# Performance work log

Hardware: AMD Instinct MI355X
Metric: run time of the kernel (lower is better)

Reference implementation:

```python
import jax, jax.numpy as jnp
import numpy as np

K_NEIGHBORS = 20


def _glorot(key, shape):
    fan_in = shape[0]
    return jax.random.normal(key, shape, dtype=jnp.float32) / jnp.sqrt(jnp.float32(fan_in))


def setup_inputs() -> dict:
    key = jax.random.key(0)
    ks = jax.random.split(key, 20)
    B, N, D = 16, 1024, 3
    out_channels = 40
    pos = jax.random.normal(ks[0], (B, N, D), dtype=jnp.float32)
    inp = {
        "pos": pos,
        # conv1 MLP: [6 -> 64 -> 64 -> 64]
        "W1a": _glorot(ks[1], (6, 64)),   "b1a": jnp.zeros((64,), jnp.float32),
        "W1b": _glorot(ks[2], (64, 64)),  "b1b": jnp.zeros((64,), jnp.float32),
        "W1c": _glorot(ks[3], (64, 64)),  "b1c": jnp.zeros((64,), jnp.float32),
        # conv2 MLP: [128 -> 128]
        "W2": _glorot(ks[4], (128, 128)), "b2": jnp.zeros((128,), jnp.float32),
        # lin1: 64+128 -> 1024
        "Wl": _glorot(ks[5], (192, 1024)), "bl": jnp.zeros((1024,), jnp.float32),
        # head MLP: [1024 -> 512 -> 256 -> out]
        "Wm1": _glorot(ks[6], (1024, 512)), "bm1": jnp.zeros((512,), jnp.float32),
        "Wm2": _glorot(ks[7], (512, 256)),  "bm2": jnp.zeros((256,), jnp.float32),
        "Wm3": _glorot(ks[8], (256, out_channels)), "bm3": jnp.zeros((out_channels,), jnp.float32),
    }
    return inp


def _knn_idx(x, k):
    # x: [B, N, D] -> idx: [B, N, k] of nearest neighbors (self excluded)
    sq = jnp.sum(x * x, axis=-1)                      # [B, N]
    d = sq[:, :, None] + sq[:, None, :] - 2.0 * jnp.einsum("bnd,bmd->bnm", x, x)
    n = x.shape[1]
    d = d + jnp.eye(n, dtype=d.dtype)[None] * jnp.float32(1e10)  # exclude self
    _, idx = jax.lax.top_k(-d, k)                     # smallest distances
    return idx


def _edge_conv(x, k, mlp_fn):
    # DynamicEdgeConv: kNN graph on current features, message = mlp([x_i, x_j - x_i]), max-aggr.
    idx = _knn_idx(x, k)                              # [B, N, k]
    nb = jax.vmap(lambda xb, ib: xb[ib])(x, idx)      # [B, N, k, C] gather
    xi = jnp.broadcast_to(x[:, :, None, :], nb.shape)
    e = jnp.concatenate([xi, nb - xi], axis=-1)       # [B, N, k, 2C]
    return jnp.max(mlp_fn(e), axis=2)                 # max over neighbors -> [B, N, C']


def reference(pos, W1a, b1a, W1b, b1b, W1c, b1c, W2, b2, Wl, bl,
              Wm1, bm1, Wm2, bm2, Wm3, bm3):
    relu = jax.nn.relu
    # conv1: MLP([6,64,64,64]) -- ReLU after hidden layers, plain last (eval: BN identity, dropout off)
    mlp1 = lambda e: relu(relu(e @ W1a + b1a) @ W1b + b1b) @ W1c + b1c
    x1 = _edge_conv(pos, K_NEIGHBORS, mlp1)           # [B, N, 64]
    # conv2: MLP([128,128]) -- single plain linear
    x2 = _edge_conv(x1, K_NEIGHBORS, lambda e: e @ W2 + b2)  # [B, N, 128]
    out = jnp.concatenate([x1, x2], axis=-1) @ Wl + bl       # [B, N, 1024]
    g = jnp.max(out, axis=1)                                  # global max pool -> [B, 1024]
    h = relu(g @ Wm1 + bm1)
    h = relu(h @ Wm2 + bm2)
    logits = h @ Wm3 + bm3                                    # [B, 40]
    return jax.nn.log_softmax(logits, axis=1)
```

## Files before the change

### kernel.cpp

```cpp
#include <hip/hip_runtime.h>

constexpr int NB  = 16;
constexpr int NP  = 1024;
constexpr int NPT = NB * NP;
constexpr int KNB = 20;

typedef unsigned short ushortT;
typedef __bf16 bf16x8 __attribute__((ext_vector_type(8)));
typedef _Float16 f16x8 __attribute__((ext_vector_type(8)));
typedef float f32x4 __attribute__((ext_vector_type(4)));

__device__ inline unsigned f2bf_pair(float f0, float f1) {
    unsigned u0 = __float_as_uint(f0); u0 = (u0 + 0x7FFFu + ((u0 >> 16) & 1u)) >> 16;
    unsigned u1 = __float_as_uint(f1); u1 = (u1 + 0x7FFFu + ((u1 >> 16) & 1u)) >> 16;
    return u0 | (u1 << 16);
}

__device__ inline unsigned monokey(float f) {
    unsigned u = __float_as_uint(f);
    return u ^ ((unsigned)((int)u >> 31) | 0x80000000u);
}

__device__ inline unsigned dppmin16(unsigned v) {
    unsigned t;
    t = (unsigned)__builtin_amdgcn_update_dpp((int)v, (int)v, 0xB1, 0xF, 0xF, false);
    v = v < t ? v : t;
    t = (unsigned)__builtin_amdgcn_update_dpp((int)v, (int)v, 0x4E, 0xF, 0xF, false);
    v = v < t ? v : t;
    t = (unsigned)__builtin_amdgcn_update_dpp((int)v, (int)v, 0x141, 0xF, 0xF, false);
    v = v < t ? v : t;
    t = (unsigned)__builtin_amdgcn_update_dpp((int)v, (int)v, 0x140, 0xF, 0xF, false);
    v = v < t ? v : t;
    return v;
}

__device__ inline void sort16_u64(unsigned long long key[16]) {
#pragma unroll
    for (int k = 2; k <= 16; k <<= 1) {
#pragma unroll
        for (int j = k >> 1; j > 0; j >>= 1) {
#pragma unroll
            for (int a = 0; a < 16; ++a) {
                int b = a ^ j;
                if (b > a) {
                    unsigned long long x = key[a], y = key[b];
                    bool lt = x < y;
                    unsigned long long mn = lt ? x : y, mx = lt ? y : x;
                    if ((a & k) == 0) { key[a] = mn; key[b] = mx; }
                    else              { key[a] = mx; key[b] = mn; }
                }
            }
        }
    }
}

__device__ inline void wave_top20_lds(unsigned long long key[16], int lane,
                                      unsigned long long* __restrict__ col,
                                      int* __restrict__ outp, int jadd)
{
    sort16_u64(key);
#pragma unroll
    for (int s = 0; s < 16; ++s) col[s] = key[s];
    unsigned ptr = 0;
    unsigned long long cur = col[0];
    unsigned long long nxt = col[1];
    for (int t = 0; t < KNB; ++t) {
        unsigned hv = (unsigned)(cur >> 32);
        unsigned hj = (unsigned)cur;
        unsigned r = dppmin16(hv);
        unsigned g0 = (unsigned)__builtin_amdgcn_readlane((int)r, 0);
        unsigned g1 = (unsigned)__builtin_amdgcn_readlane((int)r, 16);
        unsigned g2 = (unsigned)__builtin_amdgcn_readlane((int)r, 32);
        unsigned g3 = (unsigned)__builtin_amdgcn_readlane((int)r, 48);
        unsigned g = min(min(g0, g1), min(g2, g3));
        unsigned long long ball = __ballot(hv == g);
        int wl = __ffsll(ball) - 1;
        int wj = __builtin_amdgcn_readlane((int)hj, wl);
        if (lane == 0) outp[t] = jadd + wj;
        if (lane == wl) {
            cur = nxt;
            ptr += 1u;
            unsigned p2 = ptr + 1u;
            unsigned p2c = p2 < 15u ? p2 : 15u;
            unsigned long long ld = col[p2c];
            nxt = (p2 < 16u) ? ld : ~0ULL;
        }
    }
}

__global__ void fail_kernel(float* out, int n) {
    int i = blockIdx.x * 256 + threadIdx.x;
    if (i < n) out[i] = -777.0f;
}

__global__ __launch_bounds__(256) void phase1_kernel(
    const float* __restrict__ pos, const float* __restrict__ W1a, const float* __restrict__ b1a,
    const float* __restrict__ W2,
    const float* __restrict__ Wm1, const float* __restrict__ Wm2, const float* __restrict__ Wm3,
    const float* __restrict__ Wl, const float* __restrict__ W1b, const float* __restrict__ W1c,
    int* __restrict__ idx, float* __restrict__ u1, float* __restrict__ v1,
    float* __restrict__ Wcat, float* __restrict__ Wm1T, float* __restrict__ Wm2T, float* __restrict__ Wm3T,
    ushortT* __restrict__ Wlb, _Float16* __restrict__ Wc1f)
{
    __shared__ unsigned long long heap[4][64][16];
    const int bid = blockIdx.x;
    const int tid = threadIdx.x;
    if (bid < 4096) {
        const int w = tid >> 6, lane = tid & 63;
        const int b = bid >> 8;
        const int i = ((bid & 255) << 2) + w;
        const float* pb = pos + (size_t)b * NP * 3;
        float cbuf[48];
        {
            const float4* src = (const float4*)(pb + lane * 48);
#pragma unroll
            for (int q = 0; q < 12; ++q) *(float4*)&cbuf[q * 4] = src[q];
        }
        const float xi = pb[3 * i], yi = pb[3 * i + 1], zi = pb[3 * i + 2];
        const float sqi = xi * xi + yi * yi + zi * zi;
        unsigned long long key[16];
#pragma unroll
        for (int s = 0; s < 16; ++s) {
            float x = cbuf[3 * s], y = cbuf[3 * s + 1], z = cbuf[3 * s + 2];
            float d = sqi + (x * x + y * y + z * z) - 2.0f * (xi * x + yi * y + zi * z);
            int j = (lane << 4) + s;
            if (j == i) d += 1e10f;
            key[s] = ((unsigned long long)monokey(d) << 32) | (unsigned)j;
        }
        wave_top20_lds(key, lane, &heap[w][lane][0], idx + (size_t)(b * NP + i) * KNB, b * NP);
        return;
    }
    if (bid < 8192) {
        int id = (bid - 4096) * 256 + tid;
        int i = id >> 6, c = id & 63;
        float x = pos[3 * i], y = pos[3 * i + 1], z = pos[3 * i + 2];
        float wu0 = W1a[3 * 64 + c], wu1 = W1a[4 * 64 + c], wu2 = W1a[5 * 64 + c];
        float wv0 = W1a[0 * 64 + c] - wu0, wv1 = W1a[1 * 64 + c] - wu1, wv2 = W1a[2 * 64 + c] - wu2;
        u1[id] = x * wu0 + y * wu1 + z * wu2;
        v1[id] = b1a[c] + x * wv0 + y * wv1 + z * wv2;
        return;
    }
    int id = (bid - 8192) * 256 + tid;
    if (id < 64 * 256) {
        int c = id >> 8, n = id & 255;
        float wb = W2[(64 + c) * 128 + (n & 127)];
        Wcat[id] = (n < 128) ? wb : (W2[c * 128 + (n - 128)] - wb);
        return;
    }
    id -= 64 * 256;
    if (id < 512 * 1024) { int j = id >> 10, c = id & 1023; Wm1T[id] = Wm1[c * 512 + j]; return; }
    id -= 512 * 1024;
    if (id < 256 * 512)  { int j = id >> 9,  c = id & 511;  Wm2T[id] = Wm2[c * 256 + j]; return; }
    id -= 256 * 512;
    if (id < 40 * 256)   { int j = id >> 8,  c = id & 255;  Wm3T[id] = Wm3[c * 40 + j];  return; }
    id -= 40 * 256;
    if (id < 8 * 6 * 8 * 64 * 8) {
        int j = id & 7;
        int t = id >> 3;
        int lane = t & 63; t >>= 6;
        int f = t & 7; t >>= 3;
        int s = t % 6, nt = t / 6;
        int k = s * 32 + (lane >> 4) * 8 + j;
        int n = nt * 128 + f * 16 + (lane & 15);
        unsigned u = __float_as_uint(Wl[(size_t)k * 1024 + n]);
        u = (u + 0x7FFFu + ((u >> 16) & 1u)) >> 16;
        Wlb[id] = (ushortT)u;
        return;
    }
    id -= 8 * 6 * 8 * 64 * 8;
    if (id < 16384) {
        int mat = id >> 13;
        int rem = id & 8191;
        int part = rem >> 12;
        int t = rem & 4095;
        int frag = t >> 9;
        int r = t & 511;
        int lane = r >> 3, j = r & 7;
        int kf = frag >> 2, nf = frag & 3;
        int k = kf * 32 + (lane >> 4) * 8 + j;
        int n = nf * 16 + (lane & 15);
        float w = (mat ? W1c : W1b)[k * 64 + n];
        _Float16 hi = (_Float16)w;
        Wc1f[id] = part ? (_Float16)(w - (float)hi) : hi;
        return;
    }
}

__global__ __launch_bounds__(64, 1) void conv1_mfma_kernel(
    const int* __restrict__ idx, const float* __restrict__ u1, const float* __restrict__ v1,
    const _Float16* __restrict__ Wf, const float* __restrict__ b1b, const float* __restrict__ b1c,
    float* __restrict__ x1)
{
    __shared__ int idx_s[16 * 20];
    __shared__ __align__(16) float tr[16 * 68];
    __shared__ __align__(16) float xout[16 * 68];
    const int lane = threadIdx.x;
    const int row = lane & 15, ks = lane >> 4;
    const int pbase = blockIdx.x * 16;

    for (int t = lane; t < 320; t += 64) idx_s[t] = idx[(size_t)pbase * 20 + t];

    const f16x8* Wp = (const f16x8*)Wf;
    f16x8 wbh[2][4], wbl[2][4], wch[2][4], wcl[2][4];
#pragma unroll
    for (int kf = 0; kf < 2; ++kf)
#pragma unroll
        for (int nf = 0; nf < 4; ++nf) {
            int f = kf * 4 + nf;
            wbh[kf][nf] = Wp[(0 * 8 + f) * 64 + lane];
            wbl[kf][nf] = Wp[(1 * 8 + f) * 64 + lane];
            wch[kf][nf] = Wp[(2 * 8 + f) * 64 + lane];
            wcl[kf][nf] = Wp[(3 * 8 + f) * 64 + lane];
        }
    float bb[4], bc[4];
#pragma unroll
    for (int nf = 0; nf < 4; ++nf) { bb[nf] = b1b[nf * 16 + row]; bc[nf] = b1c[nf * 16 + row]; }

    const int P = pbase + row;
    float4 v1f[4];
    {
        const float4* v4a = (const float4*)(v1 + (size_t)P * 64 + ks * 8);
        v1f[0] = v4a[0]; v1f[1] = v4a[1];
        const float4* v4b = (const float4*)(v1 + (size_t)P * 64 + 32 + ks * 8);
        v1f[2] = v4b[0]; v1f[3] = v4b[1];
    }
    f32x4 xmax[4];
#pragma unroll
    for (int nf = 0; nf < 4; ++nf) xmax[nf] = (f32x4)(-3.0e38f);

    int jn = idx_s[row * 20];
    float4 un[4];
    {
        const float4* up = (const float4*)(u1 + (size_t)jn * 64 + ks * 8);
        un[0] = up[0]; un[1] = up[1];
        const float4* up2 = (const float4*)(u1 + (size_t)jn * 64 + 32 + ks * 8);
        un[2] = up2[0]; un[3] = up2[1];
    }
    for (int e = 0; e < 20; ++e) {
        float4 uc[4] = {un[0], un[1], un[2], un[3]};
        if (e < 19) {
            jn = idx_s[row * 20 + e + 1];
            const float4* up = (const float4*)(u1 + (size_t)jn * 64 + ks * 8);
            un[0] = up[0]; un[1] = up[1];
            const float4* up2 = (const float4*)(u1 + (size_t)jn * 64 + 32 + ks * 8);
            un[2] = up2[0]; un[3] = up2[1];
        }
        f32x4 c2[4];
#pragma unroll
        for (int nf = 0; nf < 4; ++nf) c2[nf] = (f32x4)(bb[nf]);
#pragma unroll
        for (int kf = 0; kf < 2; ++kf) {
            const float* uu = (const float*)&uc[kf * 2];
            const float* vv = (const float*)&v1f[kf * 2];
            f16x8 ah, al;
#pragma unroll
            for (int q = 0; q < 8; ++q) {
                float h = fmaxf(uu[q] + vv[q], 0.f);
                _Float16 hi = (_Float16)h;
                ah[q] = hi;
                al[q] = (_Float16)(h - (float)hi);
            }
#pragma unroll
            for (int nf = 0; nf < 4; ++nf) {
                c2[nf] = __builtin_amdgcn_mfma_f32_16x16x32_f16(ah, wbh[kf][nf], c2[nf], 0, 0, 0);
                c2[nf] = __builtin_amdgcn_mfma_f32_16x16x32_f16(ah, wbl[kf][nf], c2[nf], 0, 0, 0);
                c2[nf] = __builtin_amdgcn_mfma_f32_16x16x32_f16(al, wbh[kf][nf], c2[nf], 0, 0, 0);
            }
        }
#pragma unroll
        for (int nf = 0; nf < 4; ++nf)
#pragma unroll
            for (int r = 0; r < 4; ++r)
                tr[(ks * 4 + r) * 68 + nf * 16 + row] = fmaxf(c2[nf][r], 0.f);
        __builtin_amdgcn_sched_barrier(0);
        f32x4 c3[4];
#pragma unroll
        for (int nf = 0; nf < 4; ++nf) c3[nf] = (f32x4)0.0f;
#pragma unroll
        for (int kf = 0; kf < 2; ++kf) {
            float hbuf[8];
            *(float4*)&hbuf[0] = *(const float4*)&tr[row * 68 + kf * 32 + ks * 8];
            *(float4*)&hbuf[4] = *(const float4*)&tr[row * 68 + kf * 32 + ks * 8 + 4];
            f16x8 ah, al;
#pragma unroll
            for (int q = 0; q < 8; ++q) {
                _Float16 hi = (_Float16)hbuf[q];
                ah[q] = hi;
                al[q] = (_Float16)(hbuf[q] - (float)hi);
            }
#pragma unroll
            for (int nf = 0; nf < 4; ++nf) {
                c3[nf] = __builtin_amdgcn_mfma_f32_16x16x32_f16(ah, wch[kf][nf], c3[nf], 0, 0, 0);
                c3[nf] = __builtin_amdgcn_mfma_f32_16x16x32_f16(ah, wcl[kf][nf], c3[nf], 0, 0, 0);
                c3[nf] = __builtin_amdgcn_mfma_f32_16x16x32_f16(al, wch[kf][nf], c3[nf], 0, 0, 0);
            }
        }
        __builtin_amdgcn_sched_barrier(0);
#pragma unroll
        for (int nf = 0; nf < 4; ++nf) {
            xmax[nf][0] = fmaxf(xmax[nf][0], c3[nf][0]);
            xmax[nf][1] = fmaxf(xmax[nf][1], c3[nf][1]);
            xmax[nf][2] = fmaxf(xmax[nf][2], c3[nf][2]);
            xmax[nf][3] = fmaxf(xmax[nf][3], c3[nf][3]);
        }
    }
#pragma unroll
    for (int nf = 0; nf < 4; ++nf)
#pragma unroll
        for (int r = 0; r < 4; ++r)
            xout[(ks * 4 + r) * 68 + nf * 16 + row] = xmax[nf][r] + bc[nf];
    __builtin_amdgcn_sched_barrier(0);
    {
        const int r2 = lane >> 2, c0 = (lane & 3) * 16;
#pragma unroll
        for (int q = 0; q < 4; ++q) {
            float4 v = *(const float4*)&xout[r2 * 68 + c0 + q * 4];
            *(float4*)(x1 + (size_t)(pbase + r2) * 64 + c0 + q * 4) = v;
        }
    }
}

__global__ __launch_bounds__(256) void sqnorm_kernel(
    const float* __restrict__ x1, float* __restrict__ sq,
    ushortT* __restrict__ Afrag, _Float16* __restrict__ Xf)
{
    int i = blockIdx.x * 256 + threadIdx.x;
    const float4* r = (const float4*)(x1 + (size_t)i * 64);
    float c[64];
    float s = 0.f;
#pragma unroll
    for (int q = 0; q < 16; ++q) {
        float4 a = r[q];
        c[4 * q] = a.x; c[4 * q + 1] = a.y; c[4 * q + 2] = a.z; c[4 * q + 3] = a.w;
        s += a.x * a.x + a.y * a.y + a.z * a.z + a.w * a.w;
    }
    sq[i] = s;
    const size_t t = i >> 4;
#pragma unroll
    for (int cb = 0; cb < 8; ++cb) {
        uint4 pk;
        pk.x = f2bf_pair(c[8 * cb + 0], c[8 * cb + 1]);
        pk.y = f2bf_pair(c[8 * cb + 2], c[8 * cb + 3]);
        pk.z = f2bf_pair(c[8 * cb + 4], c[8 * cb + 5]);
        pk.w = f2bf_pair(c[8 * cb + 6], c[8 * cb + 7]);
        size_t af = (t * 6 + (cb >> 2)) * 512 + (size_t)((cb & 3) * 16 + (i & 15)) * 8;
        *(uint4*)(Afrag + af) = pk;
        int kf = cb >> 2;
        int lanef = ((cb & 3) << 4) + (i & 15);
        __align__(16) _Float16 hbuf[8];
        __align__(16) _Float16 lbuf[8];
#pragma unroll
        for (int q2 = 0; q2 < 8; ++q2) {
            float v = c[cb * 8 + q2];
            _Float16 hi = (_Float16)v;
            hbuf[q2] = hi;
            lbuf[q2] = (_Float16)(v - (float)hi);
        }
        *(uint4*)(Xf + ((t * 2 + kf) * 2 + 0) * 512 + (size_t)lanef * 8) = *(uint4*)hbuf;
        *(uint4*)(Xf + ((t * 2 + kf) * 2 + 1) * 512 + (size_t)lanef * 8) = *(uint4*)lbuf;
    }
}

__global__ __launch_bounds__(512, 2) void dist2sel_kernel(
    const _Float16* __restrict__ Xf, const float* __restrict__ sq, int* __restrict__ idx)
{
    __shared__ unsigned kls[16 * 1024];
    const int tid = threadIdx.x;
    const int w = tid >> 6, lane = tid & 63;
    const int b = blockIdx.x >> 6;
    const int rowtile = blockIdx.x & 63;
    const int c15 = lane & 15;
    const int rbase = (lane >> 4) * 4;

    const f16x8* Xv = (const f16x8*)Xf;
    const int tA = b * 64 + rowtile;
    f16x8 ah[2], al[2];
#pragma unroll
    for (int kf = 0; kf < 2; ++kf) {
        ah[kf] = Xv[((size_t)(tA * 2 + kf) * 2 + 0) * 64 + lane];
        al[kf] = Xv[((size_t)(tA * 2 + kf) * 2 + 1) * 64 + lane];
    }
    const float* sqb = sq + (size_t)b * NP;
    float sqi[4];
#pragma unroll
    for (int rr = 0; rr < 4; ++rr)
        sqi[rr] = sqb[rowtile * 16 + rbase + rr];

    for (int q = 0; q < 8; ++q) {
        const int ct = w * 8 + q;
        const int tB = b * 64 + ct;
        f16x8 bh0 = Xv[((size_t)(tB * 2 + 0) * 2 + 0) * 64 + lane];
        f16x8 bl0 = Xv[((size_t)(tB * 2 + 0) * 2 + 1) * 64 + lane];
        f16x8 bh1 = Xv[((size_t)(tB * 2 + 1) * 2 + 0) * 64 + lane];
        f16x8 bl1 = Xv[((size_t)(tB * 2 + 1) * 2 + 1) * 64 + lane];
        const int col = ct * 16 + c15;
        const float sqj = sqb[col];
        f32x4 acc = (f32x4)0.0f;
        acc = __builtin_amdgcn_mfma_f32_16x16x32_f16(ah[0], bh0, acc, 0, 0, 0);
        acc = __builtin_amdgcn_mfma_f32_16x16x32_f16(ah[0], bl0, acc, 0, 0, 0);
        acc = __builtin_amdgcn_mfma_f32_16x16x32_f16(al[0], bh0, acc, 0, 0, 0);
        acc = __builtin_amdgcn_mfma_f32_16x16x32_f16(ah[1], bh1, acc, 0, 0, 0);
        acc = __builtin_amdgcn_mfma_f32_16x16x32_f16(ah[1], bl1, acc, 0, 0, 0);
        acc = __builtin_amdgcn_mfma_f32_16x16x32_f16(al[1], bh1, acc, 0, 0, 0);
        const int pc = col ^ ((col >> 6) & 15);
#pragma unroll
        for (int rr = 0; rr < 4; ++rr) {
            float d = sqi[rr] + sqj - 2.0f * acc[rr];
            if (rowtile * 16 + rbase + rr == col) d += 1e10f;
            kls[(rbase + rr) * 1024 + pc] = monokey(d);
        }
    }
    __syncthreads();

    const int gb = b * NP;
    const int r0 = 2 * w, r1 = 2 * w + 1;
    unsigned* hrow0 = &kls[r0 * 1024];
    unsigned* hrow1 = &kls[r1 * 1024];
    unsigned long long perm0 = 0, perm1 = 0;
    {
        unsigned long long key[16];
#pragma unroll
        for (int s = 0; s < 16; ++s) {
            int col = (lane << 4) + s;
            int pc = col ^ ((col >> 6) & 15);
            key[s] = ((unsigned long long)kls[r0 * 1024 + pc] << 32) | (unsigned)col;
        }
        sort16_u64(key);
#pragma unroll
        for (int p = 0; p < 16; ++p) {
            hrow0[p * 64 + lane] = (unsigned)(key[p] >> 32);
            perm0 |= (unsigned long long)((unsigned)key[p] & 15u) << (4 * p);
        }
    }
    {
        unsigned long long key[16];
#pragma unroll
        for (int s = 0; s < 16; ++s) {
            int col = (lane << 4) + s;
            int pc = col ^ ((col >> 6) & 15);
            key[s] = ((unsigned long long)kls[r1 * 1024 + pc] << 32) | (unsigned)col;
        }
        sort16_u64(key);
#pragma unroll
        for (int p = 0; p < 16; ++p) {
            hrow1[p * 64 + lane] = (unsigned)(key[p] >> 32);
            perm1 |= (unsigned long long)((unsigned)key[p] & 15u) << (4 * p);
        }
    }
    unsigned ptrA = 0, ptrB = 0;
    unsigned curA = hrow0[lane], nxtA = hrow0[64 + lane];
    unsigned curB = hrow1[lane], nxtB = hrow1[64 + lane];
    unsigned csA = (unsigned)(perm0 & 15ull), nsA = (unsigned)((perm0 >> 4) & 15ull);
    unsigned csB = (unsigned)(perm1 & 15ull), nsB = (unsigned)((perm1 >> 4) & 15ull);
    int* outA = idx + (size_t)(gb + rowtile * 16 + r0) * KNB;
    int* outB = idx + (size_t)(gb + rowtile * 16 + r1) * KNB;
    for (int t = 0; t < KNB; ++t) {
        unsigned rmA = dppmin16(curA);
        unsigned rmB = dppmin16(curB);
        unsigned a0 = (unsigned)__builtin_amdgcn_readlane((int)rmA, 0);
        unsigned b0 = (unsigned)__builtin_amdgcn_readlane((int)rmB, 0);
        unsigned a1 = (unsigned)__builtin_amdgcn_readlane((int)rmA, 16);
        unsigned b1 = (unsigned)__builtin_amdgcn_readlane((int)rmB, 16);
        unsigned a2 = (unsigned)__builtin_amdgcn_readlane((int)rmA, 32);
        unsigned b2 = (unsigned)__builtin_amdgcn_readlane((int)rmB, 32);
        unsigned a3 = (unsigned)__builtin_amdgcn_readlane((int)rmA, 48);
        unsigned b3 = (unsigned)__builtin_amdgcn_readlane((int)rmB, 48);
        unsigned gA = min(min(a0, a1), min(a2, a3));
        unsigned gB = min(min(b0, b1), min(b2, b3));
        unsigned long long ballA = __ballot(curA == gA);
        unsigned long long ballB = __ballot(curB == gB);
        int wlA = __ffsll(ballA) - 1;
        int wlB = __ffsll(ballB) - 1;
        int jA = (lane << 4) + (int)csA;
        int jB = (lane << 4) + (int)csB;
        int wjA = __builtin_amdgcn_readlane(jA, wlA);
        int wjB = __builtin_amdgcn_readlane(jB, wlB);
        if (lane == 0) { outA[t] = gb + wjA; outB[t] = gb + wjB; }
        if (lane == wlA) {
            curA = nxtA; csA = nsA;
            ptrA += 1u;
            unsigned p2 = ptrA + 1u;
            unsigned p2c = p2 < 15u ? p2 : 15u;
            nsA = (unsigned)((perm0 >> (4 * (int)p2c)) & 15ull);
            nxtA = (p2 < 16u) ? hrow0[p2 * 64 + lane] : 0xFFFFFFFFu;
        }
        if (lane == wlB) {
            curB = nxtB; csB = nsB;
            ptrB += 1u;
            unsigned p2 = ptrB + 1u;
            unsigned p2c = p2 < 15u ? p2 : 15u;
            nsB = (unsigned)((perm1 >> (4 * (int)p2c)) & 15ull);
            nxtB = (p2 < 16u) ? hrow1[p2 * 64 + lane] : 0xFFFFFFFFu;
        }
    }
}

__global__ __launch_bounds__(256) void u2v2_kernel(
    const float* __restrict__ x1, const float* __restrict__ Wcat, const float* __restrict__ b2,
    float* __restrict__ u2, float* __restrict__ v2)
{
    __shared__ float aT[32][132];
    __shared__ float bW[32][132];
    const int tid = threadIdx.x;
    const int mt = blockIdx.x >> 1, nt = blockIdx.x & 1;
    const int m0 = mt << 7, n0 = nt << 7;
    const int ti = tid >> 4, tj = tid & 15;
    float acc[8][8];
#pragma unroll
    for (int a = 0; a < 8; ++a)
#pragma unroll
        for (int q = 0; q < 8; ++q) acc[a][q] = 0.f;
    for (int ct = 0; ct < 2; ++ct) {
        __syncthreads();
#pragma unroll
        for (int rep = 0; rep < 4; ++rep) {
            int f = tid + (rep << 8);
            { int r = f >> 3, q = f & 7;
              float4 v = *(const float4*)(x1 + (size_t)(m0 + r) * 64 + ct * 32 + q * 4);
              aT[4 * q + 0][r] = v.x; aT[4 * q + 1][r] = v.y; aT[4 * q + 2][r] = v.z; aT[4 * q + 3][r] = v.w; }
            { int cc = f >> 5, q = f & 31;
              *(float4*)&bW[cc][4 * q] = *(const float4*)(Wcat + (size_t)(ct * 32 + cc) * 256 + n0 + q * 4); }
        }
        __syncthreads();
#pragma unroll 4
        for (int c = 0; c < 32; ++c) {
            float af[8], bf[8];
            *(float4*)&af[0] = *(const float4*)&aT[c][ti * 8];
            *(float4*)&af[4] = *(const float4*)&aT[c][ti * 8 + 4];
            *(float4*)&bf[0] = *(const float4*)&bW[c][tj * 8];
            *(float4*)&bf[4] = *(const float4*)&bW[c][tj * 8 + 4];
#pragma unroll
            for (int a = 0; a < 8; ++a)
#pragma unroll
                for (int q = 0; q < 8; ++q) acc[a][q] = fmaf(af[a], bf[q], acc[a][q]);
        }
    }
#pragma unroll
    for (int a = 0; a < 8; ++a) {
        int m = m0 + ti * 8 + a;
        if (n0 < 128) {
            float outv[8];
#pragma unroll
            for (int q = 0; q < 8; ++q) outv[q] = acc[a][q];
            *(float4*)(u2 + (size_t)m * 128 + n0 + tj * 8)     = *(float4*)&outv[0];
            *(float4*)(u2 + (size_t)m * 128 + n0 + tj * 8 + 4) = *(float4*)&outv[4];
        } else {
            float outv[8];
#pragma unroll
            for (int q = 0; q < 8; ++q) outv[q] = acc[a][q] + b2[n0 - 128 + tj * 8 + q];
            *(float4*)(v2 + (size_t)m * 128 + (n0 - 128) + tj * 8)     = *(float4*)&outv[0];
            *(float4*)(v2 + (size_t)m * 128 + (n0 - 128) + tj * 8 + 4) = *(float4*)&outv[4];
        }
    }
}

__global__ __launch_bounds__(256) void gatherfrag_kernel(
    const int* __restrict__ idx, const float* __restrict__ u2,
    const float* __restrict__ v2, ushortT* __restrict__ Afrag)
{
    const int tid = threadIdx.x;
    const int i = blockIdx.x * 16 + (tid >> 4);
    const int cb = tid & 15;
    const int* ib = idx + (size_t)i * KNB;
    float m[8];
#pragma unroll
    for (int d = 0; d < 8; ++d) m[d] = -3e38f;
    for (int e = 0; e < KNB; ++e) {
        int j = ib[e];
        const float4* p = (const float4*)(u2 + (size_t)j * 128 + cb * 8);
        float4 a = p[0], b = p[1];
        m[0] = fmaxf(m[0], a.x); m[1] = fmaxf(m[1], a.y); m[2] = fmaxf(m[2], a.z); m[3] = fmaxf(m[3], a.w);
        m[4] = fmaxf(m[4], b.x); m[5] = fmaxf(m[5], b.y); m[6] = fmaxf(m[6], b.z); m[7] = fmaxf(m[7], b.w);
    }
    const float4* vp = (const float4*)(v2 + (size_t)i * 128 + cb * 8);
    float4 va = vp[0], vb = vp[1];
    m[0] += va.x; m[1] += va.y; m[2] += va.z; m[3] += va.w;
    m[4] += vb.x; m[5] += vb.y; m[6] += vb.z; m[7] += vb.w;
    uint4 pk;
    pk.x = f2bf_pair(m[0], m[1]);
    pk.y = f2bf_pair(m[2], m[3]);
    pk.z = f2bf_pair(m[4], m[5]);
    pk.w = f2bf_pair(m[6], m[7]);
    size_t af = ((size_t)(i >> 4) * 6 + 2 + (cb >> 2)) * 512 + (size_t)((cb & 3) * 16 + (i & 15)) * 8;
    *(uint4*)(Afrag + af) = pk;
}

__global__ __launch_bounds__(256) void lin1max_mfma_kernel(
    const ushortT* __restrict__ Afrag, const ushortT* __restrict__ Wlb, float* __restrict__ gp)
{
    __shared__ float red[4][128];
    const int tid = threadIdx.x;
    const int w = tid >> 6, lane = tid & 63;
    const int nt = blockIdx.x & 7;
    const int rt = (blockIdx.x >> 3) & 7;
    const int b  = blockIdx.x >> 6;
    const int rt16 = ((b << 3) + rt) * 8 + (w << 1);
    const bf16x8* Ap = (const bf16x8*)Afrag;
    const bf16x8* Bp = (const bf16x8*)Wlb;
    f32x4 acc[2][8];
#pragma unroll
    for (int mm = 0; mm < 2; ++mm)
#pragma unroll
        for (int f = 0; f < 8; ++f) acc[mm][f] = (f32x4)0.0f;
#pragma unroll
    for (int s = 0; s < 6; ++s) {
        bf16x8 a0 = Ap[((rt16    ) * 6 + s) * 64 + lane];
        bf16x8 a1 = Ap[((rt16 + 1) * 6 + s) * 64 + lane];
#pragma unroll
        for (int f = 0; f < 8; ++f) {
            bf16x8 bb = Bp[(((nt * 6 + s) << 3) + f) * 64 + lane];
            acc[0][f] = __builtin_amdgcn_mfma_f32_16x16x32_bf16(a0, bb, acc[0][f], 0, 0, 0);
            acc[1][f] = __builtin_amdgcn_mfma_f32_16x16x32_bf16(a1, bb, acc[1][f], 0, 0, 0);
        }
    }
#pragma unroll
    for (int f = 0; f < 8; ++f) {
        float m = acc[0][f][0];
        m = fmaxf(m, acc[0][f][1]); m = fmaxf(m, acc[0][f][2]); m = fmaxf(m, acc[0][f][3]);
        m = fmaxf(m, acc[1][f][0]); m = fmaxf(m, acc[1][f][1]);
        m = fmaxf(m, acc[1][f][2]); m = fmaxf(m, acc[1][f][3]);
        m = fmaxf(m, __shfl_xor(m, 16, 64));
        m = fmaxf(m, __shfl_xor(m, 32, 64));
        if (lane < 16) red[w][f * 16 + lane] = m;
    }
    __syncthreads();
    if (tid < 128) {
        float m = fmaxf(fmaxf(red[0][tid], red[1][tid]), fmaxf(red[2][tid], red[3][tid]));
        gp[((size_t)rt * NB + b) * 1024 + nt * 128 + tid] = m;
    }
}

__global__ __launch_bounds__(256) void gmax_kernel(
    const float* __restrict__ gp, const float* __restrict__ bl, float* __restrict__ gs)
{
    int id = blockIdx.x * 256 + threadIdx.x;
    int b = id >> 10, c = id & 1023;
    float m = gp[(size_t)b * 1024 + c];
#pragma unroll
    for (int part = 1; part < 8; ++part)
        m = fmaxf(m, gp[((size_t)part * NB + b) * 1024 + c]);
    gs[(size_t)b * 1024 + c] = m + bl[c];
}

__global__ __launch_bounds__(256) void head1_kernel(
    const float* __restrict__ gs, const float* __restrict__ Wm1T, const float* __restrict__ bm1,
    float* __restrict__ h1)
{
    __shared__ float red[16][17];
    const int j = blockIdx.x;
    const int t = threadIdx.x;
    const int b = t >> 4, seg = t & 15;
    const float4* wr = (const float4*)(Wm1T + (size_t)j * 1024 + seg * 64);
    const float4* gr = (const float4*)(gs + (size_t)b * 1024 + seg * 64);
    float acc = 0.f;
#pragma unroll
    for (int q = 0; q < 16; ++q) {
        float4 w = wr[q], g = gr[q];
        acc = fmaf(w.x, g.x, acc); acc = fmaf(w.y, g.y, acc);
        acc = fmaf(w.z, g.z, acc); acc = fmaf(w.w, g.w, acc);
    }
    red[b][seg] = acc;
    __syncthreads();
    if (t < 16) {
        float s = 0.f;
#pragma unroll
        for (int k = 0; k < 16; ++k) s += red[t][k];
        h1[(size_t)t * 512 + j] = fmaxf(s + bm1[j], 0.f);
    }
}

__global__ __launch_bounds__(256) void head2_kernel(
    const float* __restrict__ h1, const float* __restrict__ Wm2T, const float* __restrict__ bm2,
    float* __restrict__ h2)
{
    __shared__ float red[16][17];
    const int j = blockIdx.x;
    const int t = threadIdx.x;
    const int b = t >> 4, seg = t & 15;
    const float4* wr = (const float4*)(Wm2T + (size_t)j * 512 + seg * 32);
    const float4* hr = (const float4*)(h1 + (size_t)b * 512 + seg * 32);
    float acc = 0.f;
#pragma unroll
    for (int q = 0; q < 8; ++q) {
        float4 w = wr[q], g = hr[q];
        acc = fmaf(w.x, g.x, acc); acc = fmaf(w.y, g.y, acc);
        acc = fmaf(w.z, g.z, acc); acc = fmaf(w.w, g.w, acc);
    }
    red[b][seg] = acc;
    __syncthreads();
    if (t < 16) {
        float s = 0.f;
#pragma unroll
        for (int k = 0; k < 16; ++k) s += red[t][k];
        h2[(size_t)t * 256 + j] = fmaxf(s + bm2[j], 0.f);
    }
}

__global__ __launch_bounds__(256) void head3_kernel(
    const float* __restrict__ h2, const float* __restrict__ Wm3T, const float* __restrict__ bm3,
    float* __restrict__ out)
{
    __shared__ float lg[64];
    const int tid = threadIdx.x;
    const int b = blockIdx.x;
    if (tid < 40) {
        float acc = bm3[tid];
        const float4* wr = (const float4*)(Wm3T + (size_t)tid * 256);
        const float4* hr = (const float4*)(h2 + (size_t)b * 256);
#pragma unroll
        for (int c4 = 0; c4 < 64; ++c4) {
            float4 w = wr[c4];
            float4 g4 = hr[c4];
            acc = fmaf(w.x, g4.x, acc); acc = fmaf(w.y, g4.y, acc);
            acc = fmaf(w.z, g4.z, acc); acc = fmaf(w.w, g4.w, acc);
        }
        lg[tid] = acc;
    }
    __syncthreads();
    if (tid < 64) {
        float v = (tid < 40) ? lg[tid] : -3e38f;
        float m = v;
        for (int off = 32; off; off >>= 1) m = fmaxf(m, __shfl_xor(m, off, 64));
        float ex = (tid < 40) ? expf(v - m) : 0.f;
        float s = ex;
        for (int off = 32; off; off >>= 1) s += __shfl_xor(s, off, 64);
        if (tid < 40) out[b * 40 + tid] = v - m - logf(s);
    }
}

extern "C" void kernel_launch(void* const* d_in, const int* in_sizes, int n_in,
                              void* d_out, int out_size, void* d_ws, size_t ws_size,
                              hipStream_t stream)
{
    const float* pos = (const float*)d_in[0];
    const float* W1a = (const float*)d_in[1];
    const float* b1a = (const float*)d_in[2];
    const float* W1b = (const float*)d_in[3];
    const float* b1b = (const float*)d_in[4];
    const float* W1c = (const float*)d_in[5];
    const float* b1c = (const float*)d_in[6];
    const float* W2  = (const float*)d_in[7];
    const float* b2  = (const float*)d_in[8];
    const float* Wl  = (const float*)d_in[9];
    const float* bl  = (const float*)d_in[10];
    const float* Wm1 = (const float*)d_in[11];
    const float* bm1 = (const float*)d_in[12];
    const float* Wm2 = (const float*)d_in[13];
    const float* bm2 = (const float*)d_in[14];
    const float* Wm3 = (const float*)d_in[15];
    const float* bm3 = (const float*)d_in[16];
    float* out = (float*)d_out;

    char* ws = (char*)d_ws;
    const size_t MB = 1024 * 1024;
    size_t off = 0;
    auto alloc = [&](size_t bytes) { size_t o = off; off += (bytes + 255) & ~(size_t)255; return o; };
    size_t u2_off  = alloc(8 * MB);
    size_t v2_off  = alloc(8 * MB);
    size_t x1_off  = alloc(4 * MB);
    size_t idx_off = alloc((size_t)NPT * KNB * 4);
    size_t sq_off  = alloc((size_t)NPT * 4);
    size_t gp_off  = alloc((size_t)8 * NB * 1024 * 4);
    size_t gs_off  = alloc((size_t)NB * 1024 * 4);
    size_t h1_off  = alloc((size_t)NB * 512 * 4);
    size_t h2_off  = alloc((size_t)NB * 256 * 4);
    size_t wc_off  = alloc(64 * 256 * 4);
    size_t w1t_off = alloc(512 * 1024 * 4);
    size_t w2t_off = alloc(256 * 512 * 4);
    size_t w3t_off = alloc(40 * 256 * 4);
    size_t af_off  = alloc((size_t)(NPT / 16) * 6 * 512 * 2);
    size_t wlb_off = alloc((size_t)8 * 6 * 8 * 512 * 2);
    size_t wcf_off = alloc((size_t)16384 * 2);
    size_t xf_off  = alloc((size_t)(NPT / 16) * 2 * 2 * 512 * 2);
    if (ws_size < off) { fail_kernel<<<3, 256, 0, stream>>>(out, out_size); return; }

    float* u1    = (float*)(ws + u2_off);
    float* v1    = (float*)(ws + v2_off);
    float* u2    = (float*)(ws + u2_off);
    float* v2    = (float*)(ws + v2_off);
    float* x1    = (float*)(ws + x1_off);
    int*   idx   = (int*)(ws + idx_off);
    float* sq    = (float*)(ws + sq_off);
    float* gp    = (float*)(ws + gp_off);
    float* gs    = (float*)(ws + gs_off);
    float* h1    = (float*)(ws + h1_off);
    float* h2    = (float*)(ws + h2_off);
    float* Wcat  = (float*)(ws + wc_off);
    float* Wm1T  = (float*)(ws + w1t_off);
    float* Wm2T  = (float*)(ws + w2t_off);
    float* Wm3T  = (float*)(ws + w3t_off);
    ushortT* Afrag = (ushortT*)(ws + af_off);
    ushortT* Wlb   = (ushortT*)(ws + wlb_off);
    _Float16* Wc1f = (_Float16*)(ws + wcf_off);
    _Float16* Xf   = (_Float16*)(ws + xf_off);

    phase1_kernel<<<11688, 256, 0, stream>>>(pos, W1a, b1a, W2, Wm1, Wm2, Wm3, Wl, W1b, W1c,
                                             idx, u1, v1, Wcat, Wm1T, Wm2T, Wm3T, Wlb, Wc1f);
    conv1_mfma_kernel<<<1024, 64, 0, stream>>>(idx, u1, v1, Wc1f, b1b, b1c, x1);
    sqnorm_kernel<<<64, 256, 0, stream>>>(x1, sq, Afrag, Xf);
    dist2sel_kernel<<<1024, 512, 0, stream>>>(Xf, sq, idx);
    u2v2_kernel<<<256, 256, 0, stream>>>(x1, Wcat, b2, u2, v2);
    gatherfrag_kernel<<<1024, 256, 0, stream>>>(idx, u2, v2, Afrag);
    lin1max_mfma_kernel<<<1024, 256, 0, stream>>>(Afrag, Wlb, gp);
    gmax_kernel<<<64, 256, 0, stream>>>(gp, bl, gs);
    head1_kernel<<<512, 256, 0, stream>>>(gs, Wm1T, bm1, h1);
    head2_kernel<<<256, 256, 0, stream>>>(h1, Wm2T, bm2, h2);
    head3_kernel<<<16, 256, 0, stream>>>(h2, Wm3T, bm3, out);
}
```

Measured before the change: 192.9 us.

## Reuse dual-row 32-bit tournament top-20 selection for conv1 kNN in phase1

Factors the two-row tournament top-k loop out of the conv2 selection kernel into a shared helper, dual_tourney20. The conv1 kNN part of phase1 is reworked to use it, so each wave handles two query points with 32-bit keys plus a packed 4-bit column permutation instead of 64-bit keys, and the kNN section needs half as many blocks. This aims to cut the serial per-wave selection cost and the LDS traffic in the first kNN. The cost is more register use per wave for two rows, and a different tie-break path.

```diff
diff --git a/kernel.cpp b/kernel.cpp
--- a/kernel.cpp
+++ b/kernel.cpp
@@ -54,406 +54,16 @@
     }
 }
 
-__device__ inline void wave_top20_lds(unsigned long long key[16], int lane,
-                                      unsigned long long* __restrict__ col,
-                                      int* __restrict__ outp, int jadd)
-{
-    sort16_u64(key);
-#pragma unroll
-    for (int s = 0; s < 16; ++s) col[s] = key[s];
-    unsigned ptr = 0;
-    unsigned long long cur = col[0];
-    unsigned long long nxt = col[1];
-    for (int t = 0; t < KNB; ++t) {
-        unsigned hv = (unsigned)(cur >> 32);
-        unsigned hj = (unsigned)cur;
-        unsigned r = dppmin16(hv);
-        unsigned g0 = (unsigned)__builtin_amdgcn_readlane((int)r, 0);
-        unsigned g1 = (unsigned)__builtin_amdgcn_readlane((int)r, 16);
-        unsigned g2 = (unsigned)__builtin_amdgcn_readlane((int)r, 32);
-        unsigned g3 = (unsigned)__builtin_amdgcn_readlane((int)r, 48);
-        unsigned g = min(min(g0, g1), min(g2, g3));
-        unsigned long long ball = __ballot(hv == g);
-        int wl = __ffsll(ball) - 1;
-        int wj = __builtin_amdgcn_readlane((int)hj, wl);
-        if (lane == 0) outp[t] = jadd + wj;
-        if (lane == wl) {
-            cur = nxt;
-            ptr += 1u;
-            unsigned p2 = ptr + 1u;
-            unsigned p2c = p2 < 15u ? p2 : 15u;
-            unsigned long long ld = col[p2c];
-            nxt = (p2 < 16u) ? ld : ~0ULL;
-        }
-    }
-}
-
-__global__ void fail_kernel(float* out, int n) {
-    int i = blockIdx.x * 256 + threadIdx.x;
-    if (i < n) out[i] = -777.0f;
-}
-
-__global__ __launch_bounds__(256) void phase1_kernel(
-    const float* __restrict__ pos, const float* __restrict__ W1a, const float* __restrict__ b1a,
-    const float* __restrict__ W2,
-    const float* __restrict__ Wm1, const float* __restrict__ Wm2, const float* __restrict__ Wm3,
-    const float* __restrict__ Wl, const float* __restrict__ W1b, const float* __restrict__ W1c,
-    int* __restrict__ idx, float* __restrict__ u1, float* __restrict__ v1,
-    float* __restrict__ Wcat, float* __restrict__ Wm1T, float* __restrict__ Wm2T, float* __restrict__ Wm3T,
-    ushortT* __restrict__ Wlb, _Float16* __restrict__ Wc1f)
-{
-    __shared__ unsigned long long heap[4][64][16];
-    const int bid = blockIdx.x;
-    const int tid = threadIdx.x;
-    if (bid < 4096) {
-        const int w = tid >> 6, lane = tid & 63;
-        const int b = bid >> 8;
-        const int i = ((bid & 255) << 2) + w;
-        const float* pb = pos + (size_t)b * NP * 3;
-        float cbuf[48];
-        {
-            const float4* src = (const float4*)(pb + lane * 48);
-#pragma unroll
-            for (int q = 0; q < 12; ++q) *(float4*)&cbuf[q * 4] = src[q];
-        }
-        const float xi = pb[3 * i], yi = pb[3 * i + 1], zi = pb[3 * i + 2];
-        const float sqi = xi * xi + yi * yi + zi * zi;
-        unsigned long long key[16];
-#pragma unroll
-        for (int s = 0; s < 16; ++s) {
-            float x = cbuf[3 * s], y = cbuf[3 * s + 1], z = cbuf[3 * s + 2];
-            float d = sqi + (x * x + y * y + z * z) - 2.0f * (xi * x + yi * y + zi * z);
-            int j = (lane << 4) + s;
-            if (j == i) d += 1e10f;
-            key[s] = ((unsigned long long)monokey(d) << 32) | (unsigned)j;
-        }
-        wave_top20_lds(key, lane, &heap[w][lane][0], idx + (size_t)(b * NP + i) * KNB, b * NP);
-        return;
-    }
-    if (bid < 8192) {
-        int id = (bid - 4096) * 256 + tid;
-        int i = id >> 6, c = id & 63;
-        float x = pos[3 * i], y = pos[3 * i + 1], z = pos[3 * i + 2];
-        float wu0 = W1a[3 * 64 + c], wu1 = W1a[4 * 64 + c], wu2 = W1a[5 * 64 + c];
-        float wv0 = W1a[0 * 64 + c] - wu0, wv1 = W1a[1 * 64 + c] - wu1, wv2 = W1a[2 * 64 + c] - wu2;
-        u1[id] = x * wu0 + y * wu1 + z * wu2;
-        v1[id] = b1a[c] + x * wv0 + y * wv1 + z * wv2;
-        return;
-    }
-    int id = (bid - 8192) * 256 + tid;
-    if (id < 64 * 256) {
-        int c = id >> 8, n = id & 255;
-        float wb = W2[(64 + c) * 128 + (n & 127)];
-        Wcat[id] = (n < 128) ? wb : (W2[c * 128 + (n - 128)] - wb);
-        return;
-    }
-    id -= 64 * 256;
-    if (id < 512 * 1024) { int j = id >> 10, c = id & 1023; Wm1T[id] = Wm1[c * 512 + j]; return; }
-    id -= 512 * 1024;
-    if (id < 256 * 512)  { int j = id >> 9,  c = id & 511;  Wm2T[id] = Wm2[c * 256 + j]; return; }
-    id -= 256 * 512;
-    if (id < 40 * 256)   { int j = id >> 8,  c = id & 255;  Wm3T[id] = Wm3[c * 40 + j];  return; }
-    id -= 40 * 256;
-    if (id < 8 * 6 * 8 * 64 * 8) {
-        int j = id & 7;
-        int t = id >> 3;
-        int lane = t & 63; t >>= 6;
-        int f = t & 7; t >>= 3;
-        int s = t % 6, nt = t / 6;
-        int k = s * 32 + (lane >> 4) * 8 + j;
-        int n = nt * 128 + f * 16 + (lane & 15);
-        unsigned u = __float_as_uint(Wl[(size_t)k * 1024 + n]);
-        u = (u + 0x7FFFu + ((u >> 16) & 1u)) >> 16;
-        Wlb[id] = (ushortT)u;
-        return;
-    }
-    id -= 8 * 6 * 8 * 64 * 8;
-    if (id < 16384) {
-        int mat = id >> 13;
-        int rem = id & 8191;
-        int part = rem >> 12;
-        int t = rem & 4095;
-        int frag = t >> 9;
-        int r = t & 511;
-        int lane = r >> 3, j = r & 7;
-        int kf = frag >> 2, nf = frag & 3;
-        int k = kf * 32 + (lane >> 4) * 8 + j;
-        int n = nf * 16 + (lane & 15);
-        float w = (mat ? W1c : W1b)[k * 64 + n];
-        _Float16 hi = (_Float16)w;
-        Wc1f[id] = part ? (_Float16)(w - (float)hi) : hi;
-        return;
-    }
-}
-
-__global__ __launch_bounds__(64, 1) void conv1_mfma_kernel(
-    const int* __restrict__ idx, const float* __restrict__ u1, const float* __restrict__ v1,
-    const _Float16* __restrict__ Wf, const float* __restrict__ b1b, const float* __restrict__ b1c,
-    float* __restrict__ x1)
-{
-    __shared__ int idx_s[16 * 20];
-    __shared__ __align__(16) float tr[16 * 68];
-    __shared__ __align__(16) float xout[16 * 68];
-    const int lane = threadIdx.x;
-    const int row = lane & 15, ks = lane >> 4;
-    const int pbase = blockIdx.x * 16;
-
-    for (int t = lane; t < 320; t += 64) idx_s[t] = idx[(size_t)pbase * 20 + t];
-
-    const f16x8* Wp = (const f16x8*)Wf;
-    f16x8 wbh[2][4], wbl[2][4], wch[2][4], wcl[2][4];
-#pragma unroll
-    for (int kf = 0; kf < 2; ++kf)
-#pragma unroll
-        for (int nf = 0; nf < 4; ++nf) {
-            int f = kf * 4 + nf;
-            wbh[kf][nf] = Wp[(0 * 8 + f) * 64 + lane];
-            wbl[kf][nf] = Wp[(1 * 8 + f) * 64 + lane];
-            wch[kf][nf] = Wp[(2 * 8 + f) * 64 + lane];
-            wcl[kf][nf] = Wp[(3 * 8 + f) * 64 + lane];
-        }
-    float bb[4], bc[4];
-#pragma unroll
-    for (int nf = 0; nf < 4; ++nf) { bb[nf] = b1b[nf * 16 + row]; bc[nf] = b1c[nf * 16 + row]; }
-
-    const int P = pbase + row;
-    float4 v1f[4];
-    {
-        const float4* v4a = (const float4*)(v1 + (size_t)P * 64 + ks * 8);
-        v1f[0] = v4a[0]; v1f[1] = v4a[1];
-        const float4* v4b = (const float4*)(v1 + (size_t)P * 64 + 32 + ks * 8);
-        v1f[2] = v4b[0]; v1f[3] = v4b[1];
-    }
-    f32x4 xmax[4];
-#pragma unroll
-    for (int nf = 0; nf < 4; ++nf) xmax[nf] = (f32x4)(-3.0e38f);
-
-    int jn = idx_s[row * 20];
-    float4 un[4];
-    {
-        const float4* up = (const float4*)(u1 + (size_t)jn * 64 + ks * 8);
-        un[0] = up[0]; un[1] = up[1];
-        const float4* up2 = (const float4*)(u1 + (size_t)jn * 64 + 32 + ks * 8);
-        un[2] = up2[0]; un[3] = up2[1];
-    }
-    for (int e = 0; e < 20; ++e) {
-        float4 uc[4] = {un[0], un[1], un[2], un[3]};
-        if (e < 19) {
-            jn = idx_s[row * 20 + e + 1];
-            const float4* up = (const float4*)(u1 + (size_t)jn * 64 + ks * 8);
-            un[0] = up[0]; un[1] = up[1];
-            const float4* up2 = (const float4*)(u1 + (size_t)jn * 64 + 32 + ks * 8);
-            un[2] = up2[0]; un[3] = up2[1];
-        }
-        f32x4 c2[4];
-#pragma unroll
-        for (int nf = 0; nf < 4; ++nf) c2[nf] = (f32x4)(bb[nf]);
-#pragma unroll
-        for (int kf = 0; kf < 2; ++kf) {
-            const float* uu = (const float*)&uc[kf * 2];
-            const float* vv = (const float*)&v1f[kf * 2];
-            f16x8 ah, al;
-#pragma unroll
-            for (int q = 0; q < 8; ++q) {
-                float h = fmaxf(uu[q] + vv[q], 0.f);
-                _Float16 hi = (_Float16)h;
-                ah[q] = hi;
-                al[q] = (_Float16)(h - (float)hi);
-            }
-#pragma unroll
-            for (int nf = 0; nf < 4; ++nf) {
-                c2[nf] = __builtin_amdgcn_mfma_f32_16x16x32_f16(ah, wbh[kf][nf], c2[nf], 0, 0, 0);
-                c2[nf] = __builtin_amdgcn_mfma_f32_16x16x32_f16(ah, wbl[kf][nf], c2[nf], 0, 0, 0);
-                c2[nf] = __builtin_amdgcn_mfma_f32_16x16x32_f16(al, wbh[kf][nf], c2[nf], 0, 0, 0);
-            }
-        }
-#pragma unroll
-        for (int nf = 0; nf < 4; ++nf)
-#pragma unroll
-            for (int r = 0; r < 4; ++r)
-                tr[(ks * 4 + r) * 68 + nf * 16 + row] = fmaxf(c2[nf][r], 0.f);
-        __builtin_amdgcn_sched_barrier(0);
-        f32x4 c3[4];
-#pragma unroll
-        for (int nf = 0; nf < 4; ++nf) c3[nf] = (f32x4)0.0f;
-#pragma unroll
-        for (int kf = 0; kf < 2; ++kf) {
-            float hbuf[8];
-            *(float4*)&hbuf[0] = *(const float4*)&tr[row * 68 + kf * 32 + ks * 8];
-            *(float4*)&hbuf[4] = *(const float4*)&tr[row * 68 + kf * 32 + ks * 8 + 4];
-            f16x8 ah, al;
-#pragma unroll
-            for (int q = 0; q < 8; ++q) {
-                _Float16 hi = (_Float16)hbuf[q];
-                ah[q] = hi;
-                al[q] = (_Float16)(hbuf[q] - (float)hi);
-            }
-#pragma unroll
-            for (int nf = 0; nf < 4; ++nf) {
-                c3[nf] = __builtin_amdgcn_mfma_f32_16x16x32_f16(ah, wch[kf][nf], c3[nf], 0, 0, 0);
-                c3[nf] = __builtin_amdgcn_mfma_f32_16x16x32_f16(ah, wcl[kf][nf], c3[nf], 0, 0, 0);
-                c3[nf] = __builtin_amdgcn_mfma_f32_16x16x32_f16(al, wch[kf][nf], c3[nf], 0, 0, 0);
-            }
-        }
-        __builtin_amdgcn_sched_barrier(0);
-#pragma unroll
-        for (int nf = 0; nf < 4; ++nf) {
-            xmax[nf][0] = fmaxf(xmax[nf][0], c3[nf][0]);
-            xmax[nf][1] = fmaxf(xmax[nf][1], c3[nf][1]);
-            xmax[nf][2] = fmaxf(xmax[nf][2], c3[nf][2]);
-            xmax[nf][3] = fmaxf(xmax[nf][3], c3[nf][3]);
-        }
-    }
-#pragma unroll
-    for (int nf = 0; nf < 4; ++nf)
-#pragma unroll
-        for (int r = 0; r < 4; ++r)
-            xout[(ks * 4 + r) * 68 + nf * 16 + row] = xmax[nf][r] + bc[nf];
-    __builtin_amdgcn_sched_barrier(0);
-    {
-        const int r2 = lane >> 2, c0 = (lane & 3) * 16;
-#pragma unroll
-        for (int q = 0; q < 4; ++q) {
-            float4 v = *(const float4*)&xout[r2 * 68 + c0 + q * 4];
-            *(float4*)(x1 + (size_t)(pbase + r2) * 64 + c0 + q * 4) = v;
-        }
-    }
-}
-
-__global__ __launch_bounds__(256) void sqnorm_kernel(
-    const float* __restrict__ x1, float* __restrict__ sq,
-    ushortT* __restrict__ Afrag, _Float16* __restrict__ Xf)
-{
-    int i = blockIdx.x * 256 + threadIdx.x;
-    const float4* r = (const float4*)(x1 + (size_t)i * 64);
-    float c[64];
-    float s = 0.f;
-#pragma unroll
-    for (int q = 0; q < 16; ++q) {
-        float4 a = r[q];
-        c[4 * q] = a.x; c[4 * q + 1] = a.y; c[4 * q + 2] = a.z; c[4 * q + 3] = a.w;
-        s += a.x * a.x + a.y * a.y + a.z * a.z + a.w * a.w;
-    }
-    sq[i] = s;
-    const size_t t = i >> 4;
-#pragma unroll
-    for (int cb = 0; cb < 8; ++cb) {
-        uint4 pk;
-        pk.x = f2bf_pair(c[8 * cb + 0], c[8 * cb + 1]);
-        pk.y = f2bf_pair(c[8 * cb + 2], c[8 * cb + 3]);
-        pk.z = f2bf_pair(c[8 * cb + 4], c[8 * cb + 5]);
-        pk.w = f2bf_pair(c[8 * cb + 6], c[8 * cb + 7]);
-        size_t af = (t * 6 + (cb >> 2)) * 512 + (size_t)((cb & 3) * 16 + (i & 15)) * 8;
-        *(uint4*)(Afrag + af) = pk;
-        int kf = cb >> 2;
-        int lanef = ((cb & 3) << 4) + (i & 15);
-        __align__(16) _Float16 hbuf[8];
-        __align__(16) _Float16 lbuf[8];
-#pragma unroll
-        for (int q2 = 0; q2 < 8; ++q2) {
-            float v = c[cb * 8 + q2];
-            _Float16 hi = (_Float16)v;
-            hbuf[q2] = hi;
-            lbuf[q2] = (_Float16)(v - (float)hi);
-        }
-        *(uint4*)(Xf + ((t * 2 + kf) * 2 + 0) * 512 + (size_t)lanef * 8) = *(uint4*)hbuf;
-        *(uint4*)(Xf + ((t * 2 + kf) * 2 + 1) * 512 + (size_t)lanef * 8) = *(uint4*)lbuf;
-    }
-}
-
-__global__ __launch_bounds__(512, 2) void dist2sel_kernel(
-    const _Float16* __restrict__ Xf, const float* __restrict__ sq, int* __restrict__ idx)
-{
-    __shared__ unsigned kls[16 * 1024];
-    const int tid = threadIdx.x;
-    const int w = tid >> 6, lane = tid & 63;
-    const int b = blockIdx.x >> 6;
-    const int rowtile = blockIdx.x & 63;
-    const int c15 = lane & 15;
-    const int rbase = (lane >> 4) * 4;
-
-    const f16x8* Xv = (const f16x8*)Xf;
-    const int tA = b * 64 + rowtile;
-    f16x8 ah[2], al[2];
-#pragma unroll
-    for (int kf = 0; kf < 2; ++kf) {
-        ah[kf] = Xv[((size_t)(tA * 2 + kf) * 2 + 0) * 64 + lane];
-        al[kf] = Xv[((size_t)(tA * 2 + kf) * 2 + 1) * 64 + lane];
-    }
-    const float* sqb = sq + (size_t)b * NP;
-    float sqi[4];
-#pragma unroll
-    for (int rr = 0; rr < 4; ++rr)
-        sqi[rr] = sqb[rowtile * 16 + rbase + rr];
-
-    for (int q = 0; q < 8; ++q) {
-        const int ct = w * 8 + q;
-        const int tB = b * 64 + ct;
-        f16x8 bh0 = Xv[((size_t)(tB * 2 + 0) * 2 + 0) * 64 + lane];
-        f16x8 bl0 = Xv[((size_t)(tB * 2 + 0) * 2 + 1) * 64 + lane];
-        f16x8 bh1 = Xv[((size_t)(tB * 2 + 1) * 2 + 0) * 64 + lane];
-        f16x8 bl1 = Xv[((size_t)(tB * 2 + 1) * 2 + 1) * 64 + lane];
-        const int col = ct * 16 + c15;
-        const float sqj = sqb[col];
-        f32x4 acc = (f32x4)0.0f;
-        acc = __builtin_amdgcn_mfma_f32_16x16x32_f16(ah[0], bh0, acc, 0, 0, 0);
-        acc = __builtin_amdgcn_mfma_f32_16x16x32_f16(ah[0], bl0, acc, 0, 0, 0);
-        acc = __builtin_amdgcn_mfma_f32_16x16x32_f16(al[0], bh0, acc, 0, 0, 0);
-        acc = __builtin_amdgcn_mfma_f32_16x16x32_f16(ah[1], bh1, acc, 0, 0, 0);
-        acc = __builtin_amdgcn_mfma_f32_16x16x32_f16(ah[1], bl1, acc, 0, 0, 0);
-        acc = __builtin_amdgcn_mfma_f32_16x16x32_f16(al[1], bh1, acc, 0, 0, 0);
-        const int pc = col ^ ((col >> 6) & 15);
-#pragma unroll
-        for (int rr = 0; rr < 4; ++rr) {
-            float d = sqi[rr] + sqj - 2.0f * acc[rr];
-            if (rowtile * 16 + rbase + rr == col) d += 1e10f;
-            kls[(rbase + rr) * 1024 + pc] = monokey(d);
-        }
-    }
-    __syncthreads();
-
-    const int gb = b * NP;
-    const int r0 = 2 * w, r1 = 2 * w + 1;
-    unsigned* hrow0 = &kls[r0 * 1024];
-    unsigned* hrow1 = &kls[r1 * 1024];
-    unsigned long long perm0 = 0, perm1 = 0;
-    {
-        unsigned long long key[16];
-#pragma unroll
-        for (int s = 0; s < 16; ++s) {
-            int col = (lane << 4) + s;
-            int pc = col ^ ((col >> 6) & 15);
-            key[s] = ((unsigned long long)kls[r0 * 1024 + pc] << 32) | (unsigned)col;
-        }
-        sort16_u64(key);
-#pragma unroll
-        for (int p = 0; p < 16; ++p) {
-            hrow0[p * 64 + lane] = (unsigned)(key[p] >> 32);
-            perm0 |= (unsigned long long)((unsigned)key[p] & 15u) << (4 * p);
-        }
-    }
-    {
-        unsigned long long key[16];
-#pragma unroll
-        for (int s = 0; s < 16; ++s) {
-            int col = (lane << 4) + s;
-            int pc = col ^ ((col >> 6) & 15);
-            key[s] = ((unsigned long long)kls[r1 * 1024 + pc] << 32) | (unsigned)col;
-        }
-        sort16_u64(key);
-#pragma unroll
-        for (int p = 0; p < 16; ++p) {
-            hrow1[p * 64 + lane] = (unsigned)(key[p] >> 32);
-            perm1 |= (unsigned long long)((unsigned)key[p] & 15u) << (4 * p);
-        }
-    }
+__device__ inline void dual_tourney20(
+    unsigned* __restrict__ hrow0, unsigned long long perm0,
+    unsigned* __restrict__ hrow1, unsigned long long perm1,
+    int lane, int* __restrict__ outA, int* __restrict__ outB, int jadd)
+{
     unsigned ptrA = 0, ptrB = 0;
     unsigned curA = hrow0[lane], nxtA = hrow0[64 + lane];
     unsigned curB = hrow1[lane], nxtB = hrow1[64 + lane];
     unsigned csA = (unsigned)(perm0 & 15ull), nsA = (unsigned)((perm0 >> 4) & 15ull);
     unsigned csB = (unsigned)(perm1 & 15ull), nsB = (unsigned)((perm1 >> 4) & 15ull);
-    int* outA = idx + (size_t)(gb + rowtile * 16 + r0) * KNB;
-    int* outB = idx + (size_t)(gb + rowtile * 16 + r1) * KNB;
     for (int t = 0; t < KNB; ++t) {
         unsigned rmA = dppmin16(curA);
         unsigned rmB = dppmin16(curB);
@@ -475,7 +85,7 @@
         int jB = (lane << 4) + (int)csB;
         int wjA = __builtin_amdgcn_readlane(jA, wlA);
         int wjB = __builtin_amdgcn_readlane(jB, wlB);
-        if (lane == 0) { outA[t] = gb + wjA; outB[t] = gb + wjB; }
+        if (lane == 0) { outA[t] = jadd + wjA; outB[t] = jadd + wjB; }
         if (lane == wlA) {
             curA = nxtA; csA = nsA;
             ptrA += 1u;
@@ -493,6 +103,404 @@
             nxtB = (p2 < 16u) ? hrow1[p2 * 64 + lane] : 0xFFFFFFFFu;
         }
     }
+}
+
+__global__ void fail_kernel(float* out, int n) {
+    int i = blockIdx.x * 256 + threadIdx.x;
+    if (i < n) out[i] = -777.0f;
+}
+
+__global__ __launch_bounds__(256) void phase1_kernel(
+    const float* __restrict__ pos, const float* __restrict__ W1a, const float* __restrict__ b1a,
+    const float* __restrict__ W2,
+    const float* __restrict__ Wm1, const float* __restrict__ Wm2, const float* __restrict__ Wm3,
+    const float* __restrict__ Wl, const float* __restrict__ W1b, const float* __restrict__ W1c,
+    int* __restrict__ idx, float* __restrict__ u1, float* __restrict__ v1,
+    float* __restrict__ Wcat, float* __restrict__ Wm1T, float* __restrict__ Wm2T, float* __restrict__ Wm3T,
+    ushortT* __restrict__ Wlb, _Float16* __restrict__ Wc1f)
+{
+    __shared__ unsigned heap[4][2][1024];
+    const int bid = blockIdx.x;
+    const int tid = threadIdx.x;
+    if (bid < 2048) {
+        const int w = tid >> 6, lane = tid & 63;
+        const int b = bid >> 7;
+        const int ibase = ((bid & 127) << 3) + (w << 1);
+        const float* pb = pos + (size_t)b * NP * 3;
+        float cbuf[48];
+        {
+            const float4* src = (const float4*)(pb + lane * 48);
+#pragma unroll
+            for (int q = 0; q < 12; ++q) *(float4*)&cbuf[q * 4] = src[q];
+        }
+        unsigned* hrow0 = &heap[w][0][0];
+        unsigned* hrow1 = &heap[w][1][0];
+        unsigned long long perm0 = 0, perm1 = 0;
+        {
+            const int i = ibase;
+            const float xi = pb[3 * i], yi = pb[3 * i + 1], zi = pb[3 * i + 2];
+            const float sqi = xi * xi + yi * yi + zi * zi;
+            unsigned long long key[16];
+#pragma unroll
+            for (int s = 0; s < 16; ++s) {
+                float x = cbuf[3 * s], y = cbuf[3 * s + 1], z = cbuf[3 * s + 2];
+                float d = sqi + (x * x + y * y + z * z) - 2.0f * (xi * x + yi * y + zi * z);
+                int j = (lane << 4) + s;
+                if (j == i) d += 1e10f;
+                key[s] = ((unsigned long long)monokey(d) << 32) | (unsigned)j;
+            }
+            sort16_u64(key);
+#pragma unroll
+            for (int p = 0; p < 16; ++p) {
+                hrow0[p * 64 + lane] = (unsigned)(key[p] >> 32);
+                perm0 |= (unsigned long long)((unsigned)key[p] & 15u) << (4 * p);
+            }
+        }
+        {
+            const int i = ibase + 1;
+            const float xi = pb[3 * i], yi = pb[3 * i + 1], zi = pb[3 * i + 2];
+            const float sqi = xi * xi + yi * yi + zi * zi;
+            unsigned long long key[16];
+#pragma unroll
+            for (int s = 0; s < 16; ++s) {
+                float x = cbuf[3 * s], y = cbuf[3 * s + 1], z = cbuf[3 * s + 2];
+                float d = sqi + (x * x + y * y + z * z) - 2.0f * (xi * x + yi * y + zi * z);
+                int j = (lane << 4) + s;
+                if (j == i) d += 1e10f;
+                key[s] = ((unsigned long long)monokey(d) << 32) | (unsigned)j;
+            }
+            sort16_u64(key);
+#pragma unroll
+            for (int p = 0; p < 16; ++p) {
+                hrow1[p * 64 + lane] = (unsigned)(key[p] >> 32);
+                perm1 |= (unsigned long long)((unsigned)key[p] & 15u) << (4 * p);
+            }
+        }
+        dual_tourney20(hrow0, perm0, hrow1, perm1, lane,
+                       idx + (size_t)(b * NP + ibase) * KNB,
+                       idx + (size_t)(b * NP + ibase + 1) * KNB, b * NP);
+        return;
+    }
+    if (bid < 6144) {
+        int id = (bid - 2048) * 256 + tid;
+        int i = id >> 6, c = id & 63;
+        float x = pos[3 * i], y = pos[3 * i + 1], z = pos[3 * i + 2];
+        float wu0 = W1a[3 * 64 + c], wu1 = W1a[4 * 64 + c], wu2 = W1a[5 * 64 + c];
+        float wv0 = W1a[0 * 64 + c] - wu0, wv1 = W1a[1 * 64 + c] - wu1, wv2 = W1a[2 * 64 + c] - wu2;
+        u1[id] = x * wu0 + y * wu1 + z * wu2;
+        v1[id] = b1a[c] + x * wv0 + y * wv1 + z * wv2;
+        return;
+    }
+    int id = (bid - 6144) * 256 + tid;
+    if (id < 64 * 256) {
+        int c = id >> 8, n = id & 255;
+        float wb = W2[(64 + c) * 128 + (n & 127)];
+        Wcat[id] = (n < 128) ? wb : (W2[c * 128 + (n - 128)] - wb);
+        return;
+    }
+    id -= 64 * 256;
+    if (id < 512 * 1024) { int j = id >> 10, c = id & 1023; Wm1T[id] = Wm1[c * 512 + j]; return; }
+    id -= 512 * 1024;
+    if (id < 256 * 512)  { int j = id >> 9,  c = id & 511;  Wm2T[id] = Wm2[c * 256 + j]; return; }
+    id -= 256 * 512;
+    if (id < 40 * 256)   { int j = id >> 8,  c = id & 255;  Wm3T[id] = Wm3[c * 40 + j];  return; }
+    id -= 40 * 256;
+    if (id < 8 * 6 * 8 * 64 * 8) {
+        int j = id & 7;
+        int t = id >> 3;
+        int lane = t & 63; t >>= 6;
+        int f = t & 7; t >>= 3;
+        int s = t % 6, nt = t / 6;
+        int k = s * 32 + (lane >> 4) * 8 + j;
+        int n = nt * 128 + f * 16 + (lane & 15);
+        unsigned u = __float_as_uint(Wl[(size_t)k * 1024 + n]);
+        u = (u + 0x7FFFu + ((u >> 16) & 1u)) >> 16;
+        Wlb[id] = (ushortT)u;
+        return;
+    }
+    id -= 8 * 6 * 8 * 64 * 8;
+    if (id < 16384) {
+        int mat = id >> 13;
+        int rem = id & 8191;
+        int part = rem >> 12;
+        int t = rem & 4095;
+        int frag = t >> 9;
+        int r = t & 511;
+        int lane = r >> 3, j = r & 7;
+        int kf = frag >> 2, nf = frag & 3;
+        int k = kf * 32 + (lane >> 4) * 8 + j;
+        int n = nf * 16 + (lane & 15);
+        float w = (mat ? W1c : W1b)[k * 64 + n];
+        _Float16 hi = (_Float16)w;
+        Wc1f[id] = part ? (_Float16)(w - (float)hi) : hi;
+        return;
+    }
+}
+
+__global__ __launch_bounds__(64, 1) void conv1_mfma_kernel(
+    const int* __restrict__ idx, const float* __restrict__ u1, const float* __restrict__ v1,
+    const _Float16* __restrict__ Wf, const float* __restrict__ b1b, const float* __restrict__ b1c,
+    float* __restrict__ x1)
+{
+    __shared__ int idx_s[16 * 20];
+    __shared__ __align__(16) float tr[16 * 68];
+    __shared__ __align__(16) float xout[16 * 68];
+    const int lane = threadIdx.x;
+    const int row = lane & 15, ks = lane >> 4;
+    const int pbase = blockIdx.x * 16;
+
+    for (int t = lane; t < 320; t += 64) idx_s[t] = idx[(size_t)pbase * 20 + t];
+
+    const f16x8* Wp = (const f16x8*)Wf;
+    f16x8 wbh[2][4], wbl[2][4], wch[2][4], wcl[2][4];
+#pragma unroll
+    for (int kf = 0; kf < 2; ++kf)
+#pragma unroll
+        for (int nf = 0; nf < 4; ++nf) {
+            int f = kf * 4 + nf;
+            wbh[kf][nf] = Wp[(0 * 8 + f) * 64 + lane];
+            wbl[kf][nf] = Wp[(1 * 8 + f) * 64 + lane];
+            wch[kf][nf] = Wp[(2 * 8 + f) * 64 + lane];
+            wcl[kf][nf] = Wp[(3 * 8 + f) * 64 + lane];
+        }
+    float bb[4], bc[4];
+#pragma unroll
+    for (int nf = 0; nf < 4; ++nf) { bb[nf] = b1b[nf * 16 + row]; bc[nf] = b1c[nf * 16 + row]; }
+
+    const int P = pbase + row;
+    float4 v1f[4];
+    {
+        const float4* v4a = (const float4*)(v1 + (size_t)P * 64 + ks * 8);
+        v1f[0] = v4a[0]; v1f[1] = v4a[1];
+        const float4* v4b = (const float4*)(v1 + (size_t)P * 64 + 32 + ks * 8);
+        v1f[2] = v4b[0]; v1f[3] = v4b[1];
+    }
+    f32x4 xmax[4];
+#pragma unroll
+    for (int nf = 0; nf < 4; ++nf) xmax[nf] = (f32x4)(-3.0e38f);
+
+    int jn = idx_s[row * 20];
+    float4 un[4];
+    {
+        const float4* up = (const float4*)(u1 + (size_t)jn * 64 + ks * 8);
+        un[0] = up[0]; un[1] = up[1];
+        const float4* up2 = (const float4*)(u1 + (size_t)jn * 64 + 32 + ks * 8);
+        un[2] = up2[0]; un[3] = up2[1];
+    }
+    for (int e = 0; e < 20; ++e) {
+        float4 uc[4] = {un[0], un[1], un[2], un[3]};
+        if (e < 19) {
+            jn = idx_s[row * 20 + e + 1];
+            const float4* up = (const float4*)(u1 + (size_t)jn * 64 + ks * 8);
+            un[0] = up[0]; un[1] = up[1];
+            const float4* up2 = (const float4*)(u1 + (size_t)jn * 64 + 32 + ks * 8);
+            un[2] = up2[0]; un[3] = up2[1];
+        }
+        f32x4 c2[4];
+#pragma unroll
+        for (int nf = 0; nf < 4; ++nf) c2[nf] = (f32x4)(bb[nf]);
+#pragma unroll
+        for (int kf = 0; kf < 2; ++kf) {
+            const float* uu = (const float*)&uc[kf * 2];
+            const float* vv = (const float*)&v1f[kf * 2];
+            f16x8 ah, al;
+#pragma unroll
+            for (int q = 0; q < 8; ++q) {
+                float h = fmaxf(uu[q] + vv[q], 0.f);
+                _Float16 hi = (_Float16)h;
+                ah[q] = hi;
+                al[q] = (_Float16)(h - (float)hi);
+            }
+#pragma unroll
+            for (int nf = 0; nf < 4; ++nf) {
+                c2[nf] = __builtin_amdgcn_mfma_f32_16x16x32_f16(ah, wbh[kf][nf], c2[nf], 0, 0, 0);
+                c2[nf] = __builtin_amdgcn_mfma_f32_16x16x32_f16(ah, wbl[kf][nf], c2[nf], 0, 0, 0);
+                c2[nf] = __builtin_amdgcn_mfma_f32_16x16x32_f16(al, wbh[kf][nf], c2[nf], 0, 0, 0);
+            }
+        }
+#pragma unroll
+        for (int nf = 0; nf < 4; ++nf)
+#pragma unroll
+            for (int r = 0; r < 4; ++r)
+                tr[(ks * 4 + r) * 68 + nf * 16 + row] = fmaxf(c2[nf][r], 0.f);
+        __builtin_amdgcn_sched_barrier(0);
+        f32x4 c3[4];
+#pragma unroll
+        for (int nf = 0; nf < 4; ++nf) c3[nf] = (f32x4)0.0f;
+#pragma unroll
+        for (int kf = 0; kf < 2; ++kf) {
+            float hbuf[8];
+            *(float4*)&hbuf[0] = *(const float4*)&tr[row * 68 + kf * 32 + ks * 8];
+            *(float4*)&hbuf[4] = *(const float4*)&tr[row * 68 + kf * 32 + ks * 8 + 4];
+            f16x8 ah, al;
+#pragma unroll
+            for (int q = 0; q < 8; ++q) {
+                _Float16 hi = (_Float16)hbuf[q];
+                ah[q] = hi;
+                al[q] = (_Float16)(hbuf[q] - (float)hi);
+            }
+#pragma unroll
+            for (int nf = 0; nf < 4; ++nf) {
+                c3[nf] = __builtin_amdgcn_mfma_f32_16x16x32_f16(ah, wch[kf][nf], c3[nf], 0, 0, 0);
+                c3[nf] = __builtin_amdgcn_mfma_f32_16x16x32_f16(ah, wcl[kf][nf], c3[nf], 0, 0, 0);
+                c3[nf] = __builtin_amdgcn_mfma_f32_16x16x32_f16(al, wch[kf][nf], c3[nf], 0, 0, 0);
+            }
+        }
+        __builtin_amdgcn_sched_barrier(0);
+#pragma unroll
+        for (int nf = 0; nf < 4; ++nf) {
+            xmax[nf][0] = fmaxf(xmax[nf][0], c3[nf][0]);
+            xmax[nf][1] = fmaxf(xmax[nf][1], c3[nf][1]);
+            xmax[nf][2] = fmaxf(xmax[nf][2], c3[nf][2]);
+            xmax[nf][3] = fmaxf(xmax[nf][3], c3[nf][3]);
+        }
+    }
+#pragma unroll
+    for (int nf = 0; nf < 4; ++nf)
+#pragma unroll
+        for (int r = 0; r < 4; ++r)
+            xout[(ks * 4 + r) * 68 + nf * 16 + row] = xmax[nf][r] + bc[nf];
+    __builtin_amdgcn_sched_barrier(0);
+    {
+        const int r2 = lane >> 2, c0 = (lane & 3) * 16;
+#pragma unroll
+        for (int q = 0; q < 4; ++q) {
+            float4 v = *(const float4*)&xout[r2 * 68 + c0 + q * 4];
+            *(float4*)(x1 + (size_t)(pbase + r2) * 64 + c0 + q * 4) = v;
+        }
+    }
+}
+
+__global__ __launch_bounds__(256) void sqnorm_kernel(
+    const float* __restrict__ x1, float* __restrict__ sq,
+    ushortT* __restrict__ Afrag, _Float16* __restrict__ Xf)
+{
+    int i = blockIdx.x * 256 + threadIdx.x;
+    const float4* r = (const float4*)(x1 + (size_t)i * 64);
+    float c[64];
+    float s = 0.f;
+#pragma unroll
+    for (int q = 0; q < 16; ++q) {
+        float4 a = r[q];
+        c[4 * q] = a.x; c[4 * q + 1] = a.y; c[4 * q + 2] = a.z; c[4 * q + 3] = a.w;
+        s += a.x * a.x + a.y * a.y + a.z * a.z + a.w * a.w;
+    }
+    sq[i] = s;
+    const size_t t = i >> 4;
+#pragma unroll
+    for (int cb = 0; cb < 8; ++cb) {
+        uint4 pk;
+        pk.x = f2bf_pair(c[8 * cb + 0], c[8 * cb + 1]);
+        pk.y = f2bf_pair(c[8 * cb + 2], c[8 * cb + 3]);
+        pk.z = f2bf_pair(c[8 * cb + 4], c[8 * cb + 5]);
+        pk.w = f2bf_pair(c[8 * cb + 6], c[8 * cb + 7]);
+        size_t af = (t * 6 + (cb >> 2)) * 512 + (size_t)((cb & 3) * 16 + (i & 15)) * 8;
+        *(uint4*)(Afrag + af) = pk;
+        int kf = cb >> 2;
+        int lanef = ((cb & 3) << 4) + (i & 15);
+        __align__(16) _Float16 hbuf[8];
+        __align__(16) _Float16 lbuf[8];
+#pragma unroll
+        for (int q2 = 0; q2 < 8; ++q2) {
+            float v = c[cb * 8 + q2];
+            _Float16 hi = (_Float16)v;
+            hbuf[q2] = hi;
+            lbuf[q2] = (_Float16)(v - (float)hi);
+        }
+        *(uint4*)(Xf + ((t * 2 + kf) * 2 + 0) * 512 + (size_t)lanef * 8) = *(uint4*)hbuf;
+        *(uint4*)(Xf + ((t * 2 + kf) * 2 + 1) * 512 + (size_t)lanef * 8) = *(uint4*)lbuf;
+    }
+}
+
+__global__ __launch_bounds__(512, 2) void dist2sel_kernel(
+    const _Float16* __restrict__ Xf, const float* __restrict__ sq, int* __restrict__ idx)
+{
+    __shared__ unsigned kls[16 * 1024];
+    const int tid = threadIdx.x;
+    const int w = tid >> 6, lane = tid & 63;
+    const int b = blockIdx.x >> 6;
+    const int rowtile = blockIdx.x & 63;
+    const int c15 = lane & 15;
+    const int rbase = (lane >> 4) * 4;
+
+    const f16x8* Xv = (const f16x8*)Xf;
+    const int tA = b * 64 + rowtile;
+    f16x8 ah[2], al[2];
+#pragma unroll
+    for (int kf = 0; kf < 2; ++kf) {
+        ah[kf] = Xv[((size_t)(tA * 2 + kf) * 2 + 0) * 64 + lane];
+        al[kf] = Xv[((size_t)(tA * 2 + kf) * 2 + 1) * 64 + lane];
+    }
+    const float* sqb = sq + (size_t)b * NP;
+    float sqi[4];
+#pragma unroll
+    for (int rr = 0; rr < 4; ++rr)
+        sqi[rr] = sqb[rowtile * 16 + rbase + rr];
+
+    for (int q = 0; q < 8; ++q) {
+        const int ct = w * 8 + q;
+        const int tB = b * 64 + ct;
+        f16x8 bh0 = Xv[((size_t)(tB * 2 + 0) * 2 + 0) * 64 + lane];
+        f16x8 bl0 = Xv[((size_t)(tB * 2 + 0) * 2 + 1) * 64 + lane];
+        f16x8 bh1 = Xv[((size_t)(tB * 2 + 1) * 2 + 0) * 64 + lane];
+        f16x8 bl1 = Xv[((size_t)(tB * 2 + 1) * 2 + 1) * 64 + lane];
+        const int col = ct * 16 + c15;
+        const float sqj = sqb[col];
+        f32x4 acc = (f32x4)0.0f;
+        acc = __builtin_amdgcn_mfma_f32_16x16x32_f16(ah[0], bh0, acc, 0, 0, 0);
+        acc = __builtin_amdgcn_mfma_f32_16x16x32_f16(ah[0], bl0, acc, 0, 0, 0);
+        acc = __builtin_amdgcn_mfma_f32_16x16x32_f16(al[0], bh0, acc, 0, 0, 0);
+        acc = __builtin_amdgcn_mfma_f32_16x16x32_f16(ah[1], bh1, acc, 0, 0, 0);
+        acc = __builtin_amdgcn_mfma_f32_16x16x32_f16(ah[1], bl1, acc, 0, 0, 0);
+        acc = __builtin_amdgcn_mfma_f32_16x16x32_f16(al[1], bh1, acc, 0, 0, 0);
+        const int pc = col ^ ((col >> 6) & 15);
+#pragma unroll
+        for (int rr = 0; rr < 4; ++rr) {
+            float d = sqi[rr] + sqj - 2.0f * acc[rr];
+            if (rowtile * 16 + rbase + rr == col) d += 1e10f;
+            kls[(rbase + rr) * 1024 + pc] = monokey(d);
+        }
+    }
+    __syncthreads();
+
+    const int gb = b * NP;
+    const int r0 = 2 * w, r1 = 2 * w + 1;
+    unsigned* hrow0 = &kls[r0 * 1024];
+    unsigned* hrow1 = &kls[r1 * 1024];
+    unsigned long long perm0 = 0, perm1 = 0;
+    {
+        unsigned long long key[16];
+#pragma unroll
+        for (int s = 0; s < 16; ++s) {
+            int col = (lane << 4) + s;
+            int pc = col ^ ((col >> 6) & 15);
+            key[s] = ((unsigned long long)kls[r0 * 1024 + pc] << 32) | (unsigned)col;
+        }
+        sort16_u64(key);
+#pragma unroll
+        for (int p = 0; p < 16; ++p) {
+            hrow0[p * 64 + lane] = (unsigned)(key[p] >> 32);
+            perm0 |= (unsigned long long)((unsigned)key[p] & 15u) << (4 * p);
+        }
+    }
+    {
+        unsigned long long key[16];
+#pragma unroll
+        for (int s = 0; s < 16; ++s) {
+            int col = (lane << 4) + s;
+            int pc = col ^ ((col >> 6) & 15);
+            key[s] = ((unsigned long long)kls[r1 * 1024 + pc] << 32) | (unsigned)col;
+        }
+        sort16_u64(key);
+#pragma unroll
+        for (int p = 0; p < 16; ++p) {
+            hrow1[p * 64 + lane] = (unsigned)(key[p] >> 32);
+            perm1 |= (unsigned long long)((unsigned)key[p] & 15u) << (4 * p);
+        }
+    }
+    dual_tourney20(hrow0, perm0, hrow1, perm1, lane,
+                   idx + (size_t)(gb + rowtile * 16 + r0) * KNB,
+                   idx + (size_t)(gb + rowtile * 16 + r1) * KNB, gb);
 }
 
 __global__ __launch_bounds__(256) void u2v2_kernel(
@@ -794,8 +802,8 @@
     _Float16* Wc1f = (_Float16*)(ws + wcf_off);
     _Float16* Xf   = (_Float16*)(ws + xf_off);
 
-    phase1_kernel<<<11688, 256, 0, stream>>>(pos, W1a, b1a, W2, Wm1, Wm2, Wm3, Wl, W1b, W1c,
-                                             idx, u1, v1, Wcat, Wm1T, Wm2T, Wm3T, Wlb, Wc1f);
+    phase1_kernel<<<9640, 256, 0, stream>>>(pos, W1a, b1a, W2, Wm1, Wm2, Wm3, Wl, W1b, W1c,
+                                            idx, u1, v1, Wcat, Wm1T, Wm2T, Wm3T, Wlb, Wc1f);
     conv1_mfma_kernel<<<1024, 64, 0, stream>>>(idx, u1, v1, Wc1f, b1b, b1c, x1);
     sqnorm_kernel<<<64, 256, 0, stream>>>(x1, sq, Afrag, Xf);
     dist2sel_kernel<<<1024, 512, 0, stream>>>(Xf, sq, idx);
```

New measurement: 196.7 us. No clear change (+2.0%).
